# Optimization experiments

Hardware: AMD Instinct MI355X
Metric: run time of the kernel (lower is better)

The kernel has to match this reference:

```python
import jax, jax.numpy as jnp
import numpy as np

N_NODES = 200000
N_EVENTS = 150000
MEM_DIM = 128
RAW_DIM = 128
TIME_DIM = 128
MSG_DIM = 2 * MEM_DIM + RAW_DIM + TIME_DIM  # 512, IdentityMessage out_channels


def setup_inputs() -> dict:
    key = jax.random.key(0)
    ks = jax.random.split(key, 10)
    memory = jax.random.normal(ks[0], (N_NODES, MEM_DIM), jnp.float32)
    last_update = jax.random.randint(ks[1], (N_NODES,), 0, 1000, jnp.int32)
    src = jax.random.randint(ks[2], (N_EVENTS,), 0, N_NODES, jnp.int32)
    dst = jax.random.randint(ks[3], (N_EVENTS,), 0, N_NODES, jnp.int32)
    t = jax.random.randint(ks[4], (N_EVENTS,), 0, 100000, jnp.int32)
    raw_msg = jax.random.normal(ks[5], (N_EVENTS, RAW_DIM), jnp.float32)
    time_w = jax.random.normal(ks[6], (TIME_DIM,), jnp.float32) * 0.05
    time_b = jax.random.normal(ks[7], (TIME_DIM,), jnp.float32) * 0.05
    W_ih = jax.random.normal(ks[8], (3 * MEM_DIM, MSG_DIM), jnp.float32) * (1.0 / np.sqrt(MSG_DIM))
    W_hh = jax.random.normal(ks[9], (3 * MEM_DIM, MEM_DIM), jnp.float32) * (1.0 / np.sqrt(MEM_DIM))
    b_ih = jnp.zeros((3 * MEM_DIM,), jnp.float32)
    b_hh = jnp.zeros((3 * MEM_DIM,), jnp.float32)
    return {"memory": memory, "last_update": last_update, "src": src, "dst": dst,
            "t": t, "raw_msg": raw_msg, "time_w": time_w, "time_b": time_b,
            "W_ih": W_ih, "W_hh": W_hh, "b_ih": b_ih, "b_hh": b_hh}


def reference(memory, last_update, src, dst, t, raw_msg, time_w, time_b, W_ih, W_hh, b_ih, b_hh):
    N = memory.shape[0]

    def compute_msg(s, d):
        # t_rel = t - last_update[src]; time enc = cos(Linear(1->time_dim)(t_rel))
        t_rel = (t - last_update[s]).astype(memory.dtype)
        t_enc = jnp.cos(t_rel[:, None] * time_w[None, :] + time_b[None, :])
        # IdentityMessage: concat(mem[src], mem[dst], raw_msg, t_enc)  -> [E, MSG_DIM]
        return jnp.concatenate([memory[s], memory[d], raw_msg, t_enc], axis=-1)

    msg_s = compute_msg(src, dst)   # source-direction store
    msg_d = compute_msg(dst, src)   # destination-direction store (edges reversed)
    idx = jnp.concatenate([src, dst])          # destination node of each message
    msg = jnp.concatenate([msg_s, msg_d], axis=0)
    tt = jnp.concatenate([t, t])

    # MeanAggregator: segment-mean of messages per destination node
    sums = jax.ops.segment_sum(msg, idx, num_segments=N)
    cnt = jax.ops.segment_sum(jnp.ones_like(tt, dtype=msg.dtype), idx, num_segments=N)
    aggr = sums / jnp.maximum(cnt, 1.0)[:, None]

    # GRUCell(aggr, memory)
    gi = aggr @ W_ih.T + b_ih
    gh = memory @ W_hh.T + b_hh
    i_r, i_z, i_n = jnp.split(gi, 3, axis=-1)
    h_r, h_z, h_n = jnp.split(gh, 3, axis=-1)
    r = jax.nn.sigmoid(i_r + h_r)
    z = jax.nn.sigmoid(i_z + h_z)
    n = jnp.tanh(i_n + r * h_n)
    new_memory = (1.0 - z) * n + z * memory

    # last_update = scatter(t, idx, reduce='max') over all nodes
    new_last_update = jnp.zeros((N,), tt.dtype).at[idx].max(tt)
    return new_memory, new_last_update
```

## Files before the change

### kernel.cpp

```cpp
#include <hip/hip_runtime.h>
#include <cstdint>


#define MEMD 128
#define ACCD 384
#define MSGD 512

typedef __attribute__((ext_vector_type(8))) short bf16x8;
typedef __attribute__((ext_vector_type(2))) short bf16x2;
typedef __attribute__((ext_vector_type(4))) float f32x4;

static __device__ __forceinline__ short f2bf(float f) {
    uint32_t u = __builtin_bit_cast(uint32_t, f);
    u = (u + 0x7FFFu + ((u >> 16) & 1u)) >> 16;
    return (short)u;
}
static __device__ __forceinline__ float bf2f(short s) {
    return __builtin_bit_cast(float, ((uint32_t)(uint16_t)s) << 16);
}
static __device__ __forceinline__ uint32_t pack2bf(float a, float b) {
    return (uint32_t)(uint16_t)f2bf(a) | ((uint32_t)(uint16_t)f2bf(b) << 16);
}
static __device__ __forceinline__ void load_lds16(const void* g, void* l) {
    __builtin_amdgcn_global_load_lds(
        (const __attribute__((address_space(1))) unsigned int*)g,
        (__attribute__((address_space(3))) unsigned int*)l,
        16, 0, 0);
}

__global__ __launch_bounds__(256) void tgn_prep_mem(
    const float* __restrict__ mem, short* __restrict__ memB, int n8)
{
    const int i = blockIdx.x * 256 + threadIdx.x;
    if (i >= n8) return;
    const float4 a = *reinterpret_cast<const float4*>(mem + (size_t)i * 8);
    const float4 b = *reinterpret_cast<const float4*>(mem + (size_t)i * 8 + 4);
    bf16x8 v;
    v[0] = f2bf(a.x); v[1] = f2bf(a.y); v[2] = f2bf(a.z); v[3] = f2bf(a.w);
    v[4] = f2bf(b.x); v[5] = f2bf(b.y); v[6] = f2bf(b.z); v[7] = f2bf(b.w);
    *reinterpret_cast<bf16x8*>(memB + (size_t)i * 8) = v;
}

#define GI_SLOTS (24 * 16 * 64)
#define GH_SLOTS (24 * 4 * 64)

__global__ __launch_bounds__(256) void tgn_prep_w(
    const float* __restrict__ W_ih, const float* __restrict__ W_hh,
    bf16x8* __restrict__ Wb)
{
    const int s = blockIdx.x * 256 + threadIdx.x;
    if (s >= GI_SLOTS + GH_SLOTS) return;
    const float* src;
    if (s < GI_SLOTS) {
        const int n = s / (16 * 64), rem = s % (16 * 64);
        const int ks = rem / 64, l = rem % 64;
        const int j = n * 16 + (l & 15), k = ks * 32 + (l >> 4) * 8;
        src = W_ih + (size_t)j * MSGD + k;
    } else {
        const int s2 = s - GI_SLOTS;
        const int n = s2 / (4 * 64), rem = s2 % (4 * 64);
        const int ks = rem / 64, l = rem % 64;
        const int j = n * 16 + (l & 15), k = ks * 32 + (l >> 4) * 8;
        src = W_hh + (size_t)j * MEMD + k;
    }
    bf16x8 v;
    #pragma unroll
    for (int e = 0; e < 8; ++e) v[e] = f2bf(src[e]);
    Wb[s] = v;
}

__global__ __launch_bounds__(256) void tgn_fill(
    const int* __restrict__ src, const int* __restrict__ dst, const int* __restrict__ t,
    int* __restrict__ head, int* __restrict__ nxt, int* __restrict__ lu_new,
    int n_events)
{
    const int e = blockIdx.x * 256 + threadIdx.x;
    if (e >= n_events) return;
    const int s = src[e];
    const int d = dst[e];
    const int te = t[e];
    nxt[2 * e]     = atomicExch(head + s, 2 * e);
    nxt[2 * e + 1] = atomicExch(head + d, 2 * e + 1);
    atomicMax(lu_new + s, te);
    atomicMax(lu_new + d, te);
}

#define WPTR(NN, S) ((S) < 4 ? (Wh + (size_t)((NN) * 4 + (S)) * 64 + lane)      \
                             : (Wb + (size_t)((NN) * 16 + (S) - 4) * 64 + lane))

#define MFMA2(ACCN, BV)                                                          \
    ACCN[0] = __builtin_amdgcn_mfma_f32_16x16x32_bf16(a0, BV, ACCN[0], 0, 0, 0); \
    ACCN[1] = __builtin_amdgcn_mfma_f32_16x16x32_bf16(a1, BV, ACCN[1], 0, 0, 0);

#define STEP(S, B0, B1, B2, ACCARR)                                              \
    {                                                                            \
        const int ks_ = (S) < 4 ? (S) : (S) - 4;                                 \
        const bf16x8 a0 = Xf[(0 * 16 + ks_) * 64 + lane];                        \
        const bf16x8 a1 = Xf[(1 * 16 + ks_) * 64 + lane];                        \
        MFMA2(ACCARR[0], B0)                                                     \
        MFMA2(ACCARR[1], B1)                                                     \
        MFMA2(ACCARR[2], B2)                                                     \
    }                                                                            \
    if ((S) + 3 < 20) {                                                          \
        B0 = *WPTR(n0, (S) + 3);                                                 \
        B1 = *WPTR(n1, (S) + 3);                                                 \
        B2 = *WPTR(n2, (S) + 3);                                                 \
    }

__global__ __launch_bounds__(512, 4) void tgn_gru_fused(
    const short* __restrict__ memB, const int* __restrict__ head,
    const int* __restrict__ nxt,
    const int* __restrict__ src, const int* __restrict__ dst,
    const int* __restrict__ t, const float* __restrict__ raw_msg,
    const int* __restrict__ last_update,
    const float* __restrict__ time_w, const float* __restrict__ time_b,
    const bf16x8* __restrict__ Wb,
    const float* __restrict__ b_ih, const float* __restrict__ b_hh,
    const int* __restrict__ lu, float* __restrict__ out,
    float* __restrict__ out2, int n_nodes)
{
    __shared__ bf16x8 Xf[2 * 16 * 64];
    ushort* Xh = reinterpret_cast<ushort*>(Xf);
    uint32_t* X32 = reinterpret_cast<uint32_t*>(Xf);
    float*  Sout = reinterpret_cast<float*>(Xf);

    const int tid = threadIdx.x;
    const int lane = tid & 63;
    const int wv = tid >> 6;
    const int node0 = blockIdx.x * 32;

    const bf16x8* __restrict__ Wh = Wb + GI_SLOTS;
    const int n0 = wv, n1 = wv + 8, n2 = wv + 16;

    {
        const int m = wv >> 2, ks = wv & 3;
        const int slotbase = (m * 16 + ks) * 64;
        int node = node0 + m * 16 + (lane & 15);
        if (node >= n_nodes) node = n_nodes - 1;
        const int kbase = ks * 32 + (lane >> 4) * 8;
        load_lds16(memB + (size_t)node * MEMD + kbase, &Xf[slotbase]);
    }

    bf16x8 rA0 = *WPTR(n0, 0), rA1 = *WPTR(n1, 0), rA2 = *WPTR(n2, 0);
    bf16x8 rB0 = *WPTR(n0, 1), rB1 = *WPTR(n1, 1), rB2 = *WPTR(n2, 1);
    bf16x8 rC0 = *WPTR(n0, 2), rC1 = *WPTR(n1, 2), rC2 = *WPTR(n2, 2);

    {
        const int j0 = lane * 2;
        const float2 tw = *reinterpret_cast<const float2*>(time_w + j0);
        const float2 tb = *reinterpret_cast<const float2*>(time_b + j0);
        #pragma unroll
        for (int q = 0; q < 4; ++q) {
            const int n = node0 + wv * 4 + q;
            if (n >= n_nodes) break;
            int k = head[n];
            if (k < 0) continue;
            const float lus = (float)last_update[n];
            float am0 = 0.f, am1 = 0.f, ar0 = 0.f, ar1 = 0.f, at0 = 0.f, at1 = 0.f;
            int c = 0;
            while (k >= 0) {
                const int kn = nxt[k];
                const int e = k >> 1;
                const int other = (k & 1) ? src[e] : dst[e];
                const float te = (float)t[e];
                const float2 rw = *reinterpret_cast<const float2*>(raw_msg + (size_t)e * MEMD + j0);
                const bf16x2 mb = *reinterpret_cast<const bf16x2*>(memB + (size_t)other * MEMD + j0);
                const float dt = te - lus;
                at0 += __cosf(fmaf(dt, tw.x, tb.x));
                at1 += __cosf(fmaf(dt, tw.y, tb.y));
                ar0 += rw.x; ar1 += rw.y;
                am0 += bf2f(mb[0]); am1 += bf2f(mb[1]);
                ++c;
                k = kn;
            }
            const float inv = 1.0f / (float)c;
            const int nn_ = wv * 4 + q;
            const int mn = nn_ >> 4, nif = nn_ & 15;
            #pragma unroll
            for (int p = 0; p < 3; ++p) {
                const int cc = 128 + p * 128 + j0;
                const int ks = cc >> 5;
                const int hi = (cc >> 3) & 3;
                const int u32idx = ((mn * 16 + ks) * 64 + hi * 16 + nif) * 4 + (lane & 3);
                const float v0 = (p == 0 ? am0 : p == 1 ? ar0 : at0) * inv;
                const float v1 = (p == 0 ? am1 : p == 1 ? ar1 : at1) * inv;
                X32[u32idx] = pack2bf(v0, v1);
            }
        }
    }

    asm volatile("s_waitcnt vmcnt(0)" ::: "memory");
    __syncthreads();

    const int col = lane & 15;
    const int rgrp = lane >> 4;

    uint32_t hmask = 0;
    #pragma unroll
    for (int m = 0; m < 2; ++m)
        #pragma unroll
        for (int r = 0; r < 4; ++r) {
            const int node = node0 + m * 16 + rgrp * 4 + r;
            if (node < n_nodes && head[node] >= 0) hmask |= 1u << (m * 4 + r);
        }

    f32x4 acc_i[3][2], acc_h[3][2];
    #pragma unroll
    for (int c = 0; c < 3; ++c)
        #pragma unroll
        for (int m = 0; m < 2; ++m) {
            acc_i[c][m] = (f32x4){0.f, 0.f, 0.f, 0.f};
            acc_h[c][m] = (f32x4){0.f, 0.f, 0.f, 0.f};
        }

    STEP(0,  rA0, rA1, rA2, acc_h)
    STEP(1,  rB0, rB1, rB2, acc_h)
    STEP(2,  rC0, rC1, rC2, acc_h)
    STEP(3,  rA0, rA1, rA2, acc_h)
    STEP(4,  rB0, rB1, rB2, acc_i)
    STEP(5,  rC0, rC1, rC2, acc_i)
    STEP(6,  rA0, rA1, rA2, acc_i)
    STEP(7,  rB0, rB1, rB2, acc_i)
    STEP(8,  rC0, rC1, rC2, acc_i)
    STEP(9,  rA0, rA1, rA2, acc_i)
    STEP(10, rB0, rB1, rB2, acc_i)
    STEP(11, rC0, rC1, rC2, acc_i)
    STEP(12, rA0, rA1, rA2, acc_i)
    STEP(13, rB0, rB1, rB2, acc_i)
    STEP(14, rC0, rC1, rC2, acc_i)
    STEP(15, rA0, rA1, rA2, acc_i)
    STEP(16, rB0, rB1, rB2, acc_i)
    STEP(17, rC0, rC1, rC2, acc_i)
    STEP(18, rA0, rA1, rA2, acc_i)
    STEP(19, rB0, rB1, rB2, acc_i)

    const int jr = wv * 16 + col;
    const float bir = b_ih[jr], biz = b_ih[jr + 128], bin = b_ih[jr + 256];
    const float bhr = b_hh[jr], bhz = b_hh[jr + 128], bhn = b_hh[jr + 256];
    const int ksj = jr >> 5;
    const int sub = ((jr >> 3) & 3) * 16;
    const int elem = jr & 7;

    float rout[2][4];
    #pragma unroll
    for (int m = 0; m < 2; ++m) {
        #pragma unroll
        for (int r = 0; r < 4; ++r) {
            const bool has = (hmask >> (m * 4 + r)) & 1;
            const float gir = (has ? acc_i[0][m][r] : 0.f) + bir;
            const float giz = (has ? acc_i[1][m][r] : 0.f) + biz;
            const float gin = (has ? acc_i[2][m][r] : 0.f) + bin;
            const float ghr = acc_h[0][m][r] + bhr;
            const float ghz = acc_h[1][m][r] + bhz;
            const float ghn = acc_h[2][m][r] + bhn;
            const float rr = __fdividef(1.0f, 1.0f + __expf(-(gir + ghr)));
            const float zz = __fdividef(1.0f, 1.0f + __expf(-(giz + ghz)));
            const float targ = fmaf(rr, ghn, gin);
            const float e2v = __expf(2.0f * targ);
            const float nn = __fdividef(e2v - 1.0f, e2v + 1.0f);
            const int slot = (m * 16 + ksj) * 64 + sub + (rgrp * 4 + r);
            const float mv = bf2f((short)Xh[slot * 8 + elem]);
            rout[m][r] = (1.0f - zz) * nn + zz * mv;
        }
    }
    if (tid < 32 && node0 + tid < n_nodes) out2[node0 + tid] = (float)lu[node0 + tid];
    __syncthreads();

    #pragma unroll
    for (int m = 0; m < 2; ++m)
        #pragma unroll
        for (int r = 0; r < 4; ++r)
            Sout[(m * 16 + rgrp * 4 + r) * MEMD + jr] = rout[m][r];
    __syncthreads();

    float4* out4 = reinterpret_cast<float4*>(out + (size_t)node0 * MEMD);
    const float4* S4 = reinterpret_cast<const float4*>(Sout);
    if (node0 + 32 <= n_nodes) {
        #pragma unroll
        for (int it = 0; it < 2; ++it)
            out4[it * 512 + tid] = S4[it * 512 + tid];
    } else {
        #pragma unroll
        for (int it = 0; it < 2; ++it) {
            const int idx = it * 512 + tid;
            if (node0 + (idx >> 5) < n_nodes) out4[idx] = S4[idx];
        }
    }
}

extern "C" void kernel_launch(void* const* d_in, const int* in_sizes, int n_in,
                              void* d_out, int out_size, void* d_ws, size_t ws_size,
                              hipStream_t stream)
{
    const float* memory      = (const float*)d_in[0];
    const int*   last_update = (const int*)d_in[1];
    const int*   src         = (const int*)d_in[2];
    const int*   dst         = (const int*)d_in[3];
    const int*   t           = (const int*)d_in[4];
    const float* raw_msg     = (const float*)d_in[5];
    const float* time_w      = (const float*)d_in[6];
    const float* time_b      = (const float*)d_in[7];
    const float* W_ih        = (const float*)d_in[8];
    const float* W_hh        = (const float*)d_in[9];
    const float* b_ih        = (const float*)d_in[10];
    const float* b_hh        = (const float*)d_in[11];

    const int n_nodes  = in_sizes[0] / MEMD;
    const int n_events = in_sizes[2];

    int*   head = (int*)d_ws;
    int*   nxt  = head + n_nodes;
    int*   lu   = nxt + 2 * n_events;
    bf16x8* Wb  = (bf16x8*)(lu + n_nodes);
    short* memB = (short*)(Wb + GI_SLOTS + GH_SLOTS);

    (void)hipMemsetAsync(head, 0xFF, (size_t)n_nodes * sizeof(int), stream);
    (void)hipMemsetAsync(lu, 0, (size_t)n_nodes * sizeof(int), stream);

    tgn_prep_w<<<dim3((GI_SLOTS + GH_SLOTS + 255) / 256), dim3(256), 0, stream>>>(W_ih, W_hh, Wb);

    const int n8 = n_nodes * MEMD / 8;
    tgn_prep_mem<<<dim3((n8 + 255) / 256), dim3(256), 0, stream>>>(memory, memB, n8);

    tgn_fill<<<dim3((n_events + 255) / 256), dim3(256), 0, stream>>>(
        src, dst, t, head, nxt, lu, n_events);

    float* out2 = (float*)d_out + (size_t)n_nodes * MEMD;
    tgn_gru_fused<<<dim3((n_nodes + 31) / 32), dim3(512), 0, stream>>>(
        memB, head, nxt, src, dst, t, raw_msg, last_update, time_w, time_b,
        Wb, b_ih, b_hh, lu, (float*)d_out, out2, n_nodes);
}
```

Before: 334.3 us.

## Stage GRU weight tiles through LDS with double-buffered async loads

Weight B-fragments are no longer prefetched three steps ahead in registers. Each wave now streams them into a per-wave double-buffered LDS region with global_load_lds and explicit vmcnt waits, and reads them back from LDS before the MFMAs. The head-mask computation moves earlier so it overlaps the aggregation phase, and the output staging buffer moves to the new LDS area. This frees VGPRs that held nine prefetched vectors, but it adds 24KB of LDS per block, which may lower occupancy, and adds LDS round trips with a prefetch depth of only one step.

```diff
diff --git a/kernel.cpp b/kernel.cpp
--- a/kernel.cpp
+++ b/kernel.cpp
@@ -92,19 +92,28 @@
     ACCN[0] = __builtin_amdgcn_mfma_f32_16x16x32_bf16(a0, BV, ACCN[0], 0, 0, 0); \
     ACCN[1] = __builtin_amdgcn_mfma_f32_16x16x32_bf16(a1, BV, ACCN[1], 0, 0, 0);
 
-#define STEP(S, B0, B1, B2, ACCARR)                                              \
+#define STEP(S, ACCARR)                                                          \
     {                                                                            \
+        if ((S) + 1 < 20) {                                                      \
+            bf16x8* dst_ = Wr + (wv * 2 + (((S) + 1) & 1)) * 192;                \
+            load_lds16(WPTR(n0, (S) + 1), dst_);                                 \
+            load_lds16(WPTR(n1, (S) + 1), dst_ + 64);                            \
+            load_lds16(WPTR(n2, (S) + 1), dst_ + 128);                           \
+            asm volatile("s_waitcnt vmcnt(3)" ::: "memory");                     \
+        } else {                                                                 \
+            asm volatile("s_waitcnt vmcnt(0)" ::: "memory");                     \
+        }                                                                        \
+        __builtin_amdgcn_sched_barrier(0);                                       \
+        const bf16x8* sc_ = Wr + (wv * 2 + ((S) & 1)) * 192;                     \
         const int ks_ = (S) < 4 ? (S) : (S) - 4;                                 \
         const bf16x8 a0 = Xf[(0 * 16 + ks_) * 64 + lane];                        \
         const bf16x8 a1 = Xf[(1 * 16 + ks_) * 64 + lane];                        \
-        MFMA2(ACCARR[0], B0)                                                     \
-        MFMA2(ACCARR[1], B1)                                                     \
-        MFMA2(ACCARR[2], B2)                                                     \
-    }                                                                            \
-    if ((S) + 3 < 20) {                                                          \
-        B0 = *WPTR(n0, (S) + 3);                                                 \
-        B1 = *WPTR(n1, (S) + 3);                                                 \
-        B2 = *WPTR(n2, (S) + 3);                                                 \
+        const bf16x8 b0 = sc_[lane];                                             \
+        const bf16x8 b1 = sc_[64 + lane];                                        \
+        const bf16x8 b2 = sc_[128 + lane];                                       \
+        MFMA2(ACCARR[0], b0)                                                     \
+        MFMA2(ACCARR[1], b1)                                                     \
+        MFMA2(ACCARR[2], b2)                                                     \
     }
 
 __global__ __launch_bounds__(512, 4) void tgn_gru_fused(
@@ -120,9 +129,10 @@
     float* __restrict__ out2, int n_nodes)
 {
     __shared__ bf16x8 Xf[2 * 16 * 64];
+    __shared__ bf16x8 Wr[8 * 2 * 3 * 64];
     ushort* Xh = reinterpret_cast<ushort*>(Xf);
     uint32_t* X32 = reinterpret_cast<uint32_t*>(Xf);
-    float*  Sout = reinterpret_cast<float*>(Xf);
+    float*  Sout = reinterpret_cast<float*>(Wr);
 
     const int tid = threadIdx.x;
     const int lane = tid & 63;
@@ -141,9 +151,17 @@
         load_lds16(memB + (size_t)node * MEMD + kbase, &Xf[slotbase]);
     }
 
-    bf16x8 rA0 = *WPTR(n0, 0), rA1 = *WPTR(n1, 0), rA2 = *WPTR(n2, 0);
-    bf16x8 rB0 = *WPTR(n0, 1), rB1 = *WPTR(n1, 1), rB2 = *WPTR(n2, 1);
-    bf16x8 rC0 = *WPTR(n0, 2), rC1 = *WPTR(n1, 2), rC2 = *WPTR(n2, 2);
+    const int col = lane & 15;
+    const int rgrp = lane >> 4;
+
+    uint32_t hmask = 0;
+    #pragma unroll
+    for (int m = 0; m < 2; ++m)
+        #pragma unroll
+        for (int r = 0; r < 4; ++r) {
+            const int node = node0 + m * 16 + rgrp * 4 + r;
+            if (node < n_nodes && head[node] >= 0) hmask |= 1u << (m * 4 + r);
+        }
 
     {
         const int j0 = lane * 2;
@@ -192,17 +210,12 @@
     asm volatile("s_waitcnt vmcnt(0)" ::: "memory");
     __syncthreads();
 
-    const int col = lane & 15;
-    const int rgrp = lane >> 4;
-
-    uint32_t hmask = 0;
-    #pragma unroll
-    for (int m = 0; m < 2; ++m)
-        #pragma unroll
-        for (int r = 0; r < 4; ++r) {
-            const int node = node0 + m * 16 + rgrp * 4 + r;
-            if (node < n_nodes && head[node] >= 0) hmask |= 1u << (m * 4 + r);
-        }
+    {
+        bf16x8* dst_ = Wr + (wv * 2 + 0) * 192;
+        load_lds16(WPTR(n0, 0), dst_);
+        load_lds16(WPTR(n1, 0), dst_ + 64);
+        load_lds16(WPTR(n2, 0), dst_ + 128);
+    }
 
     f32x4 acc_i[3][2], acc_h[3][2];
     #pragma unroll
@@ -213,26 +226,26 @@
             acc_h[c][m] = (f32x4){0.f, 0.f, 0.f, 0.f};
         }
 
-    STEP(0,  rA0, rA1, rA2, acc_h)
-    STEP(1,  rB0, rB1, rB2, acc_h)
-    STEP(2,  rC0, rC1, rC2, acc_h)
-    STEP(3,  rA0, rA1, rA2, acc_h)
-    STEP(4,  rB0, rB1, rB2, acc_i)
-    STEP(5,  rC0, rC1, rC2, acc_i)
-    STEP(6,  rA0, rA1, rA2, acc_i)
-    STEP(7,  rB0, rB1, rB2, acc_i)
-    STEP(8,  rC0, rC1, rC2, acc_i)
-    STEP(9,  rA0, rA1, rA2, acc_i)
-    STEP(10, rB0, rB1, rB2, acc_i)
-    STEP(11, rC0, rC1, rC2, acc_i)
-    STEP(12, rA0, rA1, rA2, acc_i)
-    STEP(13, rB0, rB1, rB2, acc_i)
-    STEP(14, rC0, rC1, rC2, acc_i)
-    STEP(15, rA0, rA1, rA2, acc_i)
-    STEP(16, rB0, rB1, rB2, acc_i)
-    STEP(17, rC0, rC1, rC2, acc_i)
-    STEP(18, rA0, rA1, rA2, acc_i)
-    STEP(19, rB0, rB1, rB2, acc_i)
+    STEP(0,  acc_h)
+    STEP(1,  acc_h)
+    STEP(2,  acc_h)
+    STEP(3,  acc_h)
+    STEP(4,  acc_i)
+    STEP(5,  acc_i)
+    STEP(6,  acc_i)
+    STEP(7,  acc_i)
+    STEP(8,  acc_i)
+    STEP(9,  acc_i)
+    STEP(10, acc_i)
+    STEP(11, acc_i)
+    STEP(12, acc_i)
+    STEP(13, acc_i)
+    STEP(14, acc_i)
+    STEP(15, acc_i)
+    STEP(16, acc_i)
+    STEP(17, acc_i)
+    STEP(18, acc_i)
+    STEP(19, acc_i)
 
     const int jr = wv * 16 + col;
     const float bir = b_ih[jr], biz = b_ih[jr + 128], bin = b_ih[jr + 256];
```

Result: no change. 337.7 us (+1.0%).

## Drop bf16 memory precast kernel and interleave four linked-list walks per wave

Applied to the files above, without the earlier changes.

Removes the separate fp32-to-bf16 conversion pass over the full memory table. The fused kernel now reads fp32 memory directly, converting its own tile to bf16 in registers before the LDS store, and gathers neighbour rows in fp32. The per-node edge-list traversal is restructured so each wave walks four nodes' lists concurrently, giving more memory-level parallelism than the previous serial per-node loops. The hmask computation moves ahead of the gather. Neighbour gathers now move twice the bytes per element, and the interleaved walk uses more registers and adds divergence when list lengths differ.

```diff
diff --git a/kernel.cpp b/kernel.cpp
--- a/kernel.cpp
+++ b/kernel.cpp
@@ -20,25 +20,6 @@
 }
 static __device__ __forceinline__ uint32_t pack2bf(float a, float b) {
     return (uint32_t)(uint16_t)f2bf(a) | ((uint32_t)(uint16_t)f2bf(b) << 16);
-}
-static __device__ __forceinline__ void load_lds16(const void* g, void* l) {
-    __builtin_amdgcn_global_load_lds(
-        (const __attribute__((address_space(1))) unsigned int*)g,
-        (__attribute__((address_space(3))) unsigned int*)l,
-        16, 0, 0);
-}
-
-__global__ __launch_bounds__(256) void tgn_prep_mem(
-    const float* __restrict__ mem, short* __restrict__ memB, int n8)
-{
-    const int i = blockIdx.x * 256 + threadIdx.x;
-    if (i >= n8) return;
-    const float4 a = *reinterpret_cast<const float4*>(mem + (size_t)i * 8);
-    const float4 b = *reinterpret_cast<const float4*>(mem + (size_t)i * 8 + 4);
-    bf16x8 v;
-    v[0] = f2bf(a.x); v[1] = f2bf(a.y); v[2] = f2bf(a.z); v[3] = f2bf(a.w);
-    v[4] = f2bf(b.x); v[5] = f2bf(b.y); v[6] = f2bf(b.z); v[7] = f2bf(b.w);
-    *reinterpret_cast<bf16x8*>(memB + (size_t)i * 8) = v;
 }
 
 #define GI_SLOTS (24 * 16 * 64)
@@ -108,7 +89,7 @@
     }
 
 __global__ __launch_bounds__(512, 4) void tgn_gru_fused(
-    const short* __restrict__ memB, const int* __restrict__ head,
+    const float* __restrict__ mem, const int* __restrict__ head,
     const int* __restrict__ nxt,
     const int* __restrict__ src, const int* __restrict__ dst,
     const int* __restrict__ t, const float* __restrict__ raw_msg,
@@ -138,71 +119,94 @@
         int node = node0 + m * 16 + (lane & 15);
         if (node >= n_nodes) node = n_nodes - 1;
         const int kbase = ks * 32 + (lane >> 4) * 8;
-        load_lds16(memB + (size_t)node * MEMD + kbase, &Xf[slotbase]);
+        const float4 pa = *reinterpret_cast<const float4*>(mem + (size_t)node * MEMD + kbase);
+        const float4 pb = *reinterpret_cast<const float4*>(mem + (size_t)node * MEMD + kbase + 4);
+        bf16x8 xv;
+        xv[0] = f2bf(pa.x); xv[1] = f2bf(pa.y); xv[2] = f2bf(pa.z); xv[3] = f2bf(pa.w);
+        xv[4] = f2bf(pb.x); xv[5] = f2bf(pb.y); xv[6] = f2bf(pb.z); xv[7] = f2bf(pb.w);
+        Xf[slotbase + lane] = xv;
     }
 
     bf16x8 rA0 = *WPTR(n0, 0), rA1 = *WPTR(n1, 0), rA2 = *WPTR(n2, 0);
     bf16x8 rB0 = *WPTR(n0, 1), rB1 = *WPTR(n1, 1), rB2 = *WPTR(n2, 1);
     bf16x8 rC0 = *WPTR(n0, 2), rC1 = *WPTR(n1, 2), rC2 = *WPTR(n2, 2);
+
+    const int col = lane & 15;
+    const int rgrp = lane >> 4;
+
+    uint32_t hmask = 0;
+    #pragma unroll
+    for (int m = 0; m < 2; ++m)
+        #pragma unroll
+        for (int r = 0; r < 4; ++r) {
+            const int node = node0 + m * 16 + rgrp * 4 + r;
+            if (node < n_nodes && head[node] >= 0) hmask |= 1u << (m * 4 + r);
+        }
 
     {
         const int j0 = lane * 2;
         const float2 tw = *reinterpret_cast<const float2*>(time_w + j0);
         const float2 tb = *reinterpret_cast<const float2*>(time_b + j0);
+        const int nb = node0 + wv * 4;
+
+        int kq[4];
+        float lus[4];
+        float A[4][6];
+        int C[4];
         #pragma unroll
         for (int q = 0; q < 4; ++q) {
-            const int n = node0 + wv * 4 + q;
-            if (n >= n_nodes) break;
-            int k = head[n];
-            if (k < 0) continue;
-            const float lus = (float)last_update[n];
-            float am0 = 0.f, am1 = 0.f, ar0 = 0.f, ar1 = 0.f, at0 = 0.f, at1 = 0.f;
-            int c = 0;
-            while (k >= 0) {
-                const int kn = nxt[k];
-                const int e = k >> 1;
-                const int other = (k & 1) ? src[e] : dst[e];
-                const float te = (float)t[e];
-                const float2 rw = *reinterpret_cast<const float2*>(raw_msg + (size_t)e * MEMD + j0);
-                const bf16x2 mb = *reinterpret_cast<const bf16x2*>(memB + (size_t)other * MEMD + j0);
-                const float dt = te - lus;
-                at0 += __cosf(fmaf(dt, tw.x, tb.x));
-                at1 += __cosf(fmaf(dt, tw.y, tb.y));
-                ar0 += rw.x; ar1 += rw.y;
-                am0 += bf2f(mb[0]); am1 += bf2f(mb[1]);
-                ++c;
-                k = kn;
+            kq[q] = (nb + q < n_nodes) ? head[nb + q] : -1;
+            lus[q] = 0.f;
+            C[q] = 0;
+            #pragma unroll
+            for (int z = 0; z < 6; ++z) A[q][z] = 0.f;
+        }
+        #pragma unroll
+        for (int q = 0; q < 4; ++q)
+            if (kq[q] >= 0) lus[q] = (float)last_update[nb + q];
+
+        bool more = (kq[0] >= 0) | (kq[1] >= 0) | (kq[2] >= 0) | (kq[3] >= 0);
+        while (more) {
+            #pragma unroll
+            for (int q = 0; q < 4; ++q) {
+                const int k = kq[q];
+                if (k >= 0) {
+                    kq[q] = nxt[k];
+                    const int e = k >> 1;
+                    const int other = (k & 1) ? src[e] : dst[e];
+                    const float te = (float)t[e];
+                    const float2 rw = *reinterpret_cast<const float2*>(raw_msg + (size_t)e * MEMD + j0);
+                    const float2 mb = *reinterpret_cast<const float2*>(mem + (size_t)other * MEMD + j0);
+                    const float dt = te - lus[q];
+                    A[q][4] += __cosf(fmaf(dt, tw.x, tb.x));
+                    A[q][5] += __cosf(fmaf(dt, tw.y, tb.y));
+                    A[q][2] += rw.x; A[q][3] += rw.y;
+                    A[q][0] += mb.x; A[q][1] += mb.y;
+                    ++C[q];
+                }
             }
-            const float inv = 1.0f / (float)c;
-            const int nn_ = wv * 4 + q;
-            const int mn = nn_ >> 4, nif = nn_ & 15;
-            #pragma unroll
-            for (int p = 0; p < 3; ++p) {
-                const int cc = 128 + p * 128 + j0;
-                const int ks = cc >> 5;
-                const int hi = (cc >> 3) & 3;
-                const int u32idx = ((mn * 16 + ks) * 64 + hi * 16 + nif) * 4 + (lane & 3);
-                const float v0 = (p == 0 ? am0 : p == 1 ? ar0 : at0) * inv;
-                const float v1 = (p == 0 ? am1 : p == 1 ? ar1 : at1) * inv;
-                X32[u32idx] = pack2bf(v0, v1);
+            more = (kq[0] >= 0) | (kq[1] >= 0) | (kq[2] >= 0) | (kq[3] >= 0);
+        }
+
+        #pragma unroll
+        for (int q = 0; q < 4; ++q) {
+            if (C[q] > 0) {
+                const float inv = 1.0f / (float)C[q];
+                const int nn_ = wv * 4 + q;
+                const int mn = nn_ >> 4, nif = nn_ & 15;
+                #pragma unroll
+                for (int p = 0; p < 3; ++p) {
+                    const int cc = 128 + p * 128 + j0;
+                    const int ks = cc >> 5;
+                    const int hi = (cc >> 3) & 3;
+                    const int u32idx = ((mn * 16 + ks) * 64 + hi * 16 + nif) * 4 + (lane & 3);
+                    X32[u32idx] = pack2bf(A[q][p * 2] * inv, A[q][p * 2 + 1] * inv);
+                }
             }
         }
     }
 
-    asm volatile("s_waitcnt vmcnt(0)" ::: "memory");
     __syncthreads();
-
-    const int col = lane & 15;
-    const int rgrp = lane >> 4;
-
-    uint32_t hmask = 0;
-    #pragma unroll
-    for (int m = 0; m < 2; ++m)
-        #pragma unroll
-        for (int r = 0; r < 4; ++r) {
-            const int node = node0 + m * 16 + rgrp * 4 + r;
-            if (node < n_nodes && head[node] >= 0) hmask |= 1u << (m * 4 + r);
-        }
 
     f32x4 acc_i[3][2], acc_h[3][2];
     #pragma unroll
@@ -312,21 +316,17 @@
     int*   nxt  = head + n_nodes;
     int*   lu   = nxt + 2 * n_events;
     bf16x8* Wb  = (bf16x8*)(lu + n_nodes);
-    short* memB = (short*)(Wb + GI_SLOTS + GH_SLOTS);
 
     (void)hipMemsetAsync(head, 0xFF, (size_t)n_nodes * sizeof(int), stream);
     (void)hipMemsetAsync(lu, 0, (size_t)n_nodes * sizeof(int), stream);
 
     tgn_prep_w<<<dim3((GI_SLOTS + GH_SLOTS + 255) / 256), dim3(256), 0, stream>>>(W_ih, W_hh, Wb);
 
-    const int n8 = n_nodes * MEMD / 8;
-    tgn_prep_mem<<<dim3((n8 + 255) / 256), dim3(256), 0, stream>>>(memory, memB, n8);
-
     tgn_fill<<<dim3((n_events + 255) / 256), dim3(256), 0, stream>>>(
         src, dst, t, head, nxt, lu, n_events);
 
     float* out2 = (float*)d_out + (size_t)n_nodes * MEMD;
     tgn_gru_fused<<<dim3((n_nodes + 31) / 32), dim3(512), 0, stream>>>(
-        memB, head, nxt, src, dst, t, raw_msg, last_update, time_w, time_b,
+        memory, head, nxt, src, dst, t, raw_msg, last_update, time_w, time_b,
         Wb, b_ih, b_hh, lu, (float*)d_out, out2, n_nodes);
 }
```

Result: faster. 303.5 us (median of 2 runs) (-9.2%).
